# Optimization experiments

Measured on AMD Instinct MI355X. Metric: run time of the kernel, lower is better.

The kernel has to match this reference:

```python
import jax, jax.numpy as jnp
import numpy as np
import math

NUM_HEADS = 16

def setup_inputs() -> dict:
    key = jax.random.key(0)
    ks = jax.random.split(key, 5)
    d_model = 1024
    std = math.sqrt(2.0 / (d_model + d_model))
    x = jax.random.normal(ks[0], (2, 2048, d_model), dtype=jnp.float32)
    Wq = jax.random.normal(ks[1], (d_model, d_model), dtype=jnp.float32) * std
    Wk = jax.random.normal(ks[2], (d_model, d_model), dtype=jnp.float32) * std
    Wv = jax.random.normal(ks[3], (d_model, d_model), dtype=jnp.float32) * std
    Wo = jax.random.normal(ks[4], (d_model, d_model), dtype=jnp.float32) * std
    return {"x": x, "Wq": Wq, "Wk": Wk, "Wv": Wv, "Wo": Wo}

def reference(x, Wq, Wk, Wv, Wo):
    # x: [b, s, d]; W*: [d_out, d_in]
    b, s, d = x.shape
    h = NUM_HEADS
    dh = d // h
    def proj(W):
        y = jnp.einsum('bsd,ed->bse', x, W)           # [b, s, d]
        return y.reshape(b, s, h, dh).transpose(0, 2, 1, 3)  # [b, h, s, dh]
    Q, K, V = proj(Wq), proj(Wk), proj(Wv)
    scale = 1.0 / math.sqrt(dh)
    logits = jnp.einsum('bhqd,bhkd->bhqk', Q, K) * scale  # [b, h, s, s]
    causal = jnp.tril(jnp.ones((s, s), dtype=bool))
    logits = jnp.where(causal, logits, -jnp.inf)
    attn = jax.nn.softmax(logits, axis=-1)
    out = jnp.einsum('bhqk,bhkd->bhqd', attn, V)          # [b, h, s, dh]
    out = out.transpose(0, 2, 1, 3).reshape(b, s, d)
    return jnp.einsum('bsv,dv->bsd', out, Wo)
```

## Files before the change

kernel.cpp:

```cpp
#include <hip/hip_runtime.h>
#include <hip/hip_bf16.h>
#include <math.h>

typedef unsigned short ushort_t;
typedef __attribute__((ext_vector_type(8))) short bf16x8;
typedef __attribute__((ext_vector_type(4))) float f32x4;

#define MFMA16(a,b,c) __builtin_amdgcn_mfma_f32_16x16x32_bf16(a,b,c,0,0,0)
#define QSCALE 0.1803368801111204f

typedef unsigned int u32;
typedef __attribute__((address_space(1))) const u32* gp1_t;
typedef __attribute__((address_space(3))) u32* lp3_t;

__device__ __forceinline__ void async_copy16(void* l, const void* g) {
    __builtin_amdgcn_global_load_lds((gp1_t)g, (lp3_t)l, 16, 0, 0);
}

__device__ __forceinline__ ushort_t f2bf(float f) {
    unsigned u = __float_as_uint(f);
    unsigned r = u + 0x7fffu + ((u >> 16) & 1u);
    return (ushort_t)(r >> 16);
}

__global__ __launch_bounds__(256) void cvt_kernel(
    const float* __restrict__ x,  const float* __restrict__ wq,
    const float* __restrict__ wk, const float* __restrict__ wv,
    const float* __restrict__ wo, ushort_t* __restrict__ dst)
{
    size_t base = ((size_t)blockIdx.x * 256 + threadIdx.x) * 8;
    const float* src; size_t off;
    if      (base < 4194304ul) { src = x;  off = base; }
    else if (base < 5242880ul) { src = wq; off = base - 4194304ul; }
    else if (base < 6291456ul) { src = wk; off = base - 5242880ul; }
    else if (base < 7340032ul) { src = wv; off = base - 6291456ul; }
    else                       { src = wo; off = base - 7340032ul; }
    float4 a = *(const float4*)(src + off);
    float4 b = *(const float4*)(src + off + 4);
    struct alignas(16) U8 { ushort_t v[8]; } o;
    o.v[0]=f2bf(a.x); o.v[1]=f2bf(a.y); o.v[2]=f2bf(a.z); o.v[3]=f2bf(a.w);
    o.v[4]=f2bf(b.x); o.v[5]=f2bf(b.y); o.v[6]=f2bf(b.z); o.v[7]=f2bf(b.w);
    *(U8*)(dst + base) = o;
}

__global__ __launch_bounds__(256) void gemm_bt(
    const ushort_t* __restrict__ A,  const ushort_t* __restrict__ B0,
    const ushort_t* __restrict__ B1, const ushort_t* __restrict__ B2,
    ushort_t* __restrict__ Oq, ushort_t* __restrict__ Ok,
    ushort_t* __restrict__ Ovt, float* __restrict__ Of, int mode_base)
{
    __shared__ ushort_t As[128 * 64];
    __shared__ ushort_t Bs[128 * 64];
    const int t = threadIdx.x, l = t & 63, w = t >> 6;
    const int l4 = l >> 4, lm = l & 15;
    const int wr = w >> 1, wc = w & 1;
    const int n0 = blockIdx.x * 128, m0 = blockIdx.y * 128;
    const int mode = mode_base + blockIdx.z;
    const ushort_t* B = (mode == 1) ? B1 : (mode == 2) ? B2 : B0;

    f32x4 acc[4][4] = {};
    for (int kt = 0; kt < 16; ++kt) {
        const int k0 = kt * 64;
        __syncthreads();
        #pragma unroll
        for (int i = 0; i < 4; ++i) {
            const int row = i * 32 + (t >> 3);
            const int c = (t & 7) ^ (row & 7);
            async_copy16((char*)As + i * 4096 + t * 16,
                         A + (size_t)(m0 + row) * 1024 + k0 + c * 8);
            async_copy16((char*)Bs + i * 4096 + t * 16,
                         B + (size_t)(n0 + row) * 1024 + k0 + c * 8);
        }
        __syncthreads();
        #pragma unroll
        for (int ks = 0; ks < 2; ++ks) {
            bf16x8 af[4], bfr[4];
            #pragma unroll
            for (int mi = 0; mi < 4; ++mi) {
                const int row = wr * 64 + mi * 16 + lm;
                const int ch = l4 + 4 * ks;
                af[mi] = *(const bf16x8*)(As + row * 64 + ((ch ^ (row & 7)) << 3));
            }
            #pragma unroll
            for (int ni = 0; ni < 4; ++ni) {
                const int row = wc * 64 + ni * 16 + lm;
                const int ch = l4 + 4 * ks;
                bfr[ni] = *(const bf16x8*)(Bs + row * 64 + ((ch ^ (row & 7)) << 3));
            }
            #pragma unroll
            for (int mi = 0; mi < 4; ++mi)
                #pragma unroll
                for (int ni = 0; ni < 4; ++ni)
                    acc[mi][ni] = MFMA16(af[mi], bfr[ni], acc[mi][ni]);
        }
    }

    const int mb = m0 + wr * 64, nb = n0 + wc * 64;
    if (mode == 3) {
        #pragma unroll
        for (int mi = 0; mi < 4; ++mi)
            #pragma unroll
            for (int ni = 0; ni < 4; ++ni) {
                const int n = nb + ni * 16 + lm;
                const int mr = mb + mi * 16 + l4 * 4;
                #pragma unroll
                for (int r = 0; r < 4; ++r)
                    Of[(size_t)(mr + r) * 1024 + n] = acc[mi][ni][r];
            }
    } else if (mode == 2) {
        #pragma unroll
        for (int mi = 0; mi < 4; ++mi)
            #pragma unroll
            for (int ni = 0; ni < 4; ++ni) {
                const int n = nb + ni * 16 + lm;
                const int m = mb + mi * 16 + l4 * 4;
                const int b = m >> 11, s = m & 2047, h = n >> 6, d = n & 63;
                ushort4 pk;
                pk.x = f2bf(acc[mi][ni][0]); pk.y = f2bf(acc[mi][ni][1]);
                pk.z = f2bf(acc[mi][ni][2]); pk.w = f2bf(acc[mi][ni][3]);
                *(ushort4*)(Ovt + (((size_t)(b * 16 + h) * 64 + d) * 2048 + s)) = pk;
            }
    } else {
        ushort_t* O = (mode == 0) ? Oq : Ok;
        const float qs = (mode == 0) ? (float)QSCALE : 1.0f;
        #pragma unroll
        for (int mi = 0; mi < 4; ++mi)
            #pragma unroll
            for (int ni = 0; ni < 4; ++ni) {
                const int n = nb + ni * 16 + lm;
                const int h = n >> 6, d = n & 63;
                #pragma unroll
                for (int r = 0; r < 4; ++r) {
                    const int m = mb + mi * 16 + l4 * 4 + r;
                    const int b = m >> 11, s = m & 2047;
                    O[((size_t)(b * 16 + h) * 2048 + s) * 64 + d] =
                        f2bf(acc[mi][ni][r] * qs);
                }
            }
    }
}

template<bool MASK>
__device__ __forceinline__ void attn_tile(
    const ushort_t* Kbuf, const ushort_t* Vbuf, ushort_t* Pw,
    const bf16x8 (&qf)[2], const bf16x8 ones,
    f32x4 (&o)[4], f32x4& ol, float& m_run,
    int kv0, int qrow, int l4, int lm)
{
    f32x4 sf[4] = {};
    #pragma unroll
    for (int ks = 0; ks < 2; ++ks)
        #pragma unroll
        for (int cf = 0; cf < 4; ++cf) {
            const int rowK = cf * 16 + lm;
            const int ch = l4 + 4 * ks;
            bf16x8 kf = *(const bf16x8*)(Kbuf + rowK * 64 + ((ch ^ (rowK & 7)) << 3));
            sf[cf] = MFMA16(kf, qf[ks], sf[cf]);
        }

    float tmax = -1e30f;
    #pragma unroll
    for (int cf = 0; cf < 4; ++cf)
        #pragma unroll
        for (int r = 0; r < 4; ++r) {
            float v = sf[cf][r];
            if (MASK && (kv0 + cf * 16 + l4 * 4 + r > qrow)) v = -30000.f;
            sf[cf][r] = v;
            tmax = fmaxf(tmax, v);
        }
    tmax = fmaxf(tmax, __shfl_xor(tmax, 16));
    tmax = fmaxf(tmax, __shfl_xor(tmax, 32));

    if (!__all(tmax <= m_run + 8.f)) {
        const float mn = fmaxf(m_run, tmax);
        const float alpha = __builtin_amdgcn_exp2f(m_run - mn);
        #pragma unroll
        for (int df = 0; df < 4; ++df)
            #pragma unroll
            for (int r = 0; r < 4; ++r)
                o[df][r] *= alpha;
        #pragma unroll
        for (int r = 0; r < 4; ++r) ol[r] *= alpha;
        m_run = mn;
    }

    #pragma unroll
    for (int cf = 0; cf < 4; ++cf) {
        float p0 = __builtin_amdgcn_exp2f(sf[cf][0] - m_run);
        float p1 = __builtin_amdgcn_exp2f(sf[cf][1] - m_run);
        float p2 = __builtin_amdgcn_exp2f(sf[cf][2] - m_run);
        float p3 = __builtin_amdgcn_exp2f(sf[cf][3] - m_run);
        __hip_bfloat162 b01 = __float22bfloat162_rn(make_float2(p0, p1));
        __hip_bfloat162 b23 = __float22bfloat162_rn(make_float2(p2, p3));
        uint2 pkv;
        __builtin_memcpy(&pkv.x, &b01, 4);
        __builtin_memcpy(&pkv.y, &b23, 4);
        *(uint2*)&Pw[lm * 72 + cf * 16 + l4 * 4] = pkv;
    }

    #pragma unroll
    for (int ks = 0; ks < 2; ++ks) {
        bf16x8 pf = *(const bf16x8*)&Pw[lm * 72 + ks * 32 + l4 * 8];
        #pragma unroll
        for (int df = 0; df < 4; ++df) {
            const int rowV = df * 16 + lm;
            const int ch = l4 + 4 * ks;
            bf16x8 vf = *(const bf16x8*)(Vbuf + rowV * 64 + ((ch ^ (rowV & 7)) << 3));
            o[df] = MFMA16(vf, pf, o[df]);
        }
        ol = MFMA16(ones, pf, ol);
    }
}

__global__ __launch_bounds__(256) void attn_kernel(
    const ushort_t* __restrict__ Qg, const ushort_t* __restrict__ Kg,
    const ushort_t* __restrict__ Vtg, ushort_t* __restrict__ Og)
{
    __shared__ ushort_t Ks[2][64 * 64];
    __shared__ ushort_t Vs[2][64 * 64];
    __shared__ ushort_t Ps[4][16 * 72];
    const int t = threadIdx.x, l = t & 63, w = t >> 6;
    const int l4 = l >> 4, lm = l & 15;
    const int bh = blockIdx.x;
    const int qt = 31 - (int)blockIdx.y;
    const int q0 = qt * 64, q0w = q0 + w * 16;
    const int qrow = q0w + lm;

    bf16x8 qf[2];
    {
        const ushort_t* qp = Qg + ((size_t)bh * 2048 + qrow) * 64 + l4 * 8;
        qf[0] = *(const bf16x8*)qp;
        qf[1] = *(const bf16x8*)(qp + 32);
    }
    bf16x8 ones;
    #pragma unroll
    for (int i = 0; i < 8; ++i) ones[i] = (short)0x3F80;

    f32x4 o[4] = {};
    f32x4 ol = {};
    float m_run = -1e30f;

    const int nkv = qt + 1, last = nkv - 1;
    const int srow = t >> 3, scol = t & 7;
    const int stg_i = (srow >= 32), stg_row = srow & 31;
    const ushort_t* kg0 = Kg + ((size_t)bh * 2048 + srow) * 64 + (scol ^ (srow & 7)) * 8;
    const ushort_t* vg0 = Vtg + ((size_t)bh * 64 + srow) * 2048 + (scol ^ (srow & 7)) * 8;
    (void)stg_i; (void)stg_row;

    async_copy16((char*)&Ks[0][0] + t * 16, kg0);
    async_copy16((char*)&Vs[0][0] + t * 16, vg0);
    async_copy16((char*)&Ks[0][0] + 4096 + t * 16, kg0 + 32 * 64);
    async_copy16((char*)&Vs[0][0] + 4096 + t * 16, vg0 + 32 * 2048);
    __syncthreads();

    for (int kt = 0; kt < last; ++kt) {
        const int cur = kt & 1;
        const size_t koff = (size_t)(kt + 1) * 64 * 64;
        const size_t voff = (size_t)(kt + 1) * 64;
        async_copy16((char*)&Ks[cur ^ 1][0] + t * 16, kg0 + koff);
        async_copy16((char*)&Vs[cur ^ 1][0] + t * 16, vg0 + voff);
        async_copy16((char*)&Ks[cur ^ 1][0] + 4096 + t * 16, kg0 + koff + 32 * 64);
        async_copy16((char*)&Vs[cur ^ 1][0] + 4096 + t * 16, vg0 + voff + 32 * 2048);

        attn_tile<false>(&Ks[cur][0], &Vs[cur][0], &Ps[w][0],
                         qf, ones, o, ol, m_run, kt * 64, qrow, l4, lm);
        __syncthreads();
    }
    attn_tile<true>(&Ks[last & 1][0], &Vs[last & 1][0], &Ps[w][0],
                    qf, ones, o, ol, m_run, last * 64, qrow, l4, lm);

    const int b = bh >> 4, h = bh & 15;
    const float inv = 1.f / ol[0];
    #pragma unroll
    for (int df = 0; df < 4; ++df) {
        ushort4 pk4;
        pk4.x = f2bf(o[df][0] * inv); pk4.y = f2bf(o[df][1] * inv);
        pk4.z = f2bf(o[df][2] * inv); pk4.w = f2bf(o[df][3] * inv);
        *(ushort4*)&Og[((size_t)(b * 2048 + qrow)) * 1024 + h * 64 + df * 16 + l4 * 4] = pk4;
    }
}

extern "C" void kernel_launch(void* const* d_in, const int* in_sizes, int n_in,
                              void* d_out, int out_size, void* d_ws, size_t ws_size,
                              hipStream_t stream)
{
    const float* x  = (const float*)d_in[0];
    const float* Wq = (const float*)d_in[1];
    const float* Wk = (const float*)d_in[2];
    const float* Wv = (const float*)d_in[3];
    const float* Wo = (const float*)d_in[4];

    ushort_t* ws  = (ushort_t*)d_ws;
    ushort_t* xb  = ws;
    ushort_t* wqb = ws + 4194304;
    ushort_t* wkb = ws + 5242880;
    ushort_t* wvb = ws + 6291456;
    ushort_t* wob = ws + 7340032;
    ushort_t* Qw  = ws + 8388608;
    ushort_t* Kw  = ws + 12582912;
    ushort_t* Vtw = ws + 16777216;
    ushort_t* Aow = ws + 20971520;

    cvt_kernel<<<4096, 256, 0, stream>>>(x, Wq, Wk, Wv, Wo, ws);
    gemm_bt<<<dim3(8, 32, 3), 256, 0, stream>>>(xb, wqb, wkb, wvb,
                                                Qw, Kw, Vtw, nullptr, 0);
    attn_kernel<<<dim3(32, 32), 256, 0, stream>>>(Qw, Kw, Vtw, Aow);
    gemm_bt<<<dim3(8, 32, 1), 256, 0, stream>>>(Aow, wob, wob, wob,
                                                nullptr, nullptr, nullptr,
                                                (float*)d_out, 3);
}
```

Measured before the change: 123.7 us.

## Double-buffer GEMM LDS tiles, fuse QKV weights as one N=3072 GEMM, swizzle blocks

The GEMM now double-buffers its A/B LDS tiles, issuing async global-to-LDS loads for the next K slice while MFMAs consume the current one, and needs one barrier per iteration instead of two. The QKV projection treats the three contiguous bf16 weight matrices as a single 3072-row B operand, and picks the output destination from the column offset instead of using blockIdx.z. A block-index swizzle spreads neighbouring workgroups across chunks of the grid to improve L2 reuse. LDS use doubles to 64KB per block, which may reduce occupancy. The single barrier may leave a race: the prefetch into the other buffer is issued before the async loads of the current buffer are confirmed complete.

After: 120.2 us. 2.8% less time.

```diff
diff --git a/kernel.cpp b/kernel.cpp
--- a/kernel.cpp
+++ b/kernel.cpp
@@ -44,34 +44,52 @@
 }
 
 __global__ __launch_bounds__(256) void gemm_bt(
-    const ushort_t* __restrict__ A,  const ushort_t* __restrict__ B0,
-    const ushort_t* __restrict__ B1, const ushort_t* __restrict__ B2,
+    const ushort_t* __restrict__ A, const ushort_t* __restrict__ B,
     ushort_t* __restrict__ Oq, ushort_t* __restrict__ Ok,
-    ushort_t* __restrict__ Ovt, float* __restrict__ Of, int mode_base)
-{
-    __shared__ ushort_t As[128 * 64];
-    __shared__ ushort_t Bs[128 * 64];
+    ushort_t* __restrict__ Ovt, float* __restrict__ Of, int is_out)
+{
+    __shared__ ushort_t As[2][128 * 64];
+    __shared__ ushort_t Bs[2][128 * 64];
     const int t = threadIdx.x, l = t & 63, w = t >> 6;
     const int l4 = l >> 4, lm = l & 15;
     const int wr = w >> 1, wc = w & 1;
-    const int n0 = blockIdx.x * 128, m0 = blockIdx.y * 128;
-    const int mode = mode_base + blockIdx.z;
-    const ushort_t* B = (mode == 1) ? B1 : (mode == 2) ? B2 : B0;
+
+    const int nwg = gridDim.x * gridDim.y;
+    const int orig = (int)blockIdx.y * gridDim.x + (int)blockIdx.x;
+    const int qq = nwg >> 3;
+    const int swz = (orig & 7) * qq + (orig >> 3);
+    const int n0 = (swz % gridDim.x) * 128;
+    const int m0 = (swz / gridDim.x) * 128;
+
+    const int srow = t >> 3, scol = t & 7;
 
     f32x4 acc[4][4] = {};
+
+    #pragma unroll
+    for (int i = 0; i < 4; ++i) {
+        const int row = i * 32 + srow;
+        const int c = scol ^ (row & 7);
+        async_copy16((char*)&As[0][0] + i * 4096 + t * 16,
+                     A + (size_t)(m0 + row) * 1024 + c * 8);
+        async_copy16((char*)&Bs[0][0] + i * 4096 + t * 16,
+                     B + (size_t)(n0 + row) * 1024 + c * 8);
+    }
+    __syncthreads();
+
     for (int kt = 0; kt < 16; ++kt) {
-        const int k0 = kt * 64;
-        __syncthreads();
-        #pragma unroll
-        for (int i = 0; i < 4; ++i) {
-            const int row = i * 32 + (t >> 3);
-            const int c = (t & 7) ^ (row & 7);
-            async_copy16((char*)As + i * 4096 + t * 16,
-                         A + (size_t)(m0 + row) * 1024 + k0 + c * 8);
-            async_copy16((char*)Bs + i * 4096 + t * 16,
-                         B + (size_t)(n0 + row) * 1024 + k0 + c * 8);
-        }
-        __syncthreads();
+        const int cur = kt & 1;
+        if (kt + 1 < 16) {
+            const int k0 = (kt + 1) * 64;
+            #pragma unroll
+            for (int i = 0; i < 4; ++i) {
+                const int row = i * 32 + srow;
+                const int c = scol ^ (row & 7);
+                async_copy16((char*)&As[cur ^ 1][0] + i * 4096 + t * 16,
+                             A + (size_t)(m0 + row) * 1024 + k0 + c * 8);
+                async_copy16((char*)&Bs[cur ^ 1][0] + i * 4096 + t * 16,
+                             B + (size_t)(n0 + row) * 1024 + k0 + c * 8);
+            }
+        }
         #pragma unroll
         for (int ks = 0; ks < 2; ++ks) {
             bf16x8 af[4], bfr[4];
@@ -79,13 +97,13 @@
             for (int mi = 0; mi < 4; ++mi) {
                 const int row = wr * 64 + mi * 16 + lm;
                 const int ch = l4 + 4 * ks;
-                af[mi] = *(const bf16x8*)(As + row * 64 + ((ch ^ (row & 7)) << 3));
+                af[mi] = *(const bf16x8*)(&As[cur][0] + row * 64 + ((ch ^ (row & 7)) << 3));
             }
             #pragma unroll
             for (int ni = 0; ni < 4; ++ni) {
                 const int row = wc * 64 + ni * 16 + lm;
                 const int ch = l4 + 4 * ks;
-                bfr[ni] = *(const bf16x8*)(Bs + row * 64 + ((ch ^ (row & 7)) << 3));
+                bfr[ni] = *(const bf16x8*)(&Bs[cur][0] + row * 64 + ((ch ^ (row & 7)) << 3));
             }
             #pragma unroll
             for (int mi = 0; mi < 4; ++mi)
@@ -93,10 +111,11 @@
                 for (int ni = 0; ni < 4; ++ni)
                     acc[mi][ni] = MFMA16(af[mi], bfr[ni], acc[mi][ni]);
         }
+        __syncthreads();
     }
 
     const int mb = m0 + wr * 64, nb = n0 + wc * 64;
-    if (mode == 3) {
+    if (is_out) {
         #pragma unroll
         for (int mi = 0; mi < 4; ++mi)
             #pragma unroll
@@ -107,27 +126,28 @@
                 for (int r = 0; r < 4; ++r)
                     Of[(size_t)(mr + r) * 1024 + n] = acc[mi][ni][r];
             }
-    } else if (mode == 2) {
+    } else if (nb >= 2048) {
         #pragma unroll
         for (int mi = 0; mi < 4; ++mi)
             #pragma unroll
             for (int ni = 0; ni < 4; ++ni) {
-                const int n = nb + ni * 16 + lm;
+                const int nv = nb - 2048 + ni * 16 + lm;
                 const int m = mb + mi * 16 + l4 * 4;
-                const int b = m >> 11, s = m & 2047, h = n >> 6, d = n & 63;
+                const int b = m >> 11, s = m & 2047, h = nv >> 6, d = nv & 63;
                 ushort4 pk;
                 pk.x = f2bf(acc[mi][ni][0]); pk.y = f2bf(acc[mi][ni][1]);
                 pk.z = f2bf(acc[mi][ni][2]); pk.w = f2bf(acc[mi][ni][3]);
                 *(ushort4*)(Ovt + (((size_t)(b * 16 + h) * 64 + d) * 2048 + s)) = pk;
             }
     } else {
-        ushort_t* O = (mode == 0) ? Oq : Ok;
-        const float qs = (mode == 0) ? (float)QSCALE : 1.0f;
+        ushort_t* O = (nb < 1024) ? Oq : Ok;
+        const float qs = (nb < 1024) ? (float)QSCALE : 1.0f;
+        const int nbase = nb & 1023;
         #pragma unroll
         for (int mi = 0; mi < 4; ++mi)
             #pragma unroll
             for (int ni = 0; ni < 4; ++ni) {
-                const int n = nb + ni * 16 + lm;
+                const int n = nbase + ni * 16 + lm;
                 const int h = n >> 6, d = n & 63;
                 #pragma unroll
                 for (int r = 0; r < 4; ++r) {
@@ -242,10 +262,8 @@
 
     const int nkv = qt + 1, last = nkv - 1;
     const int srow = t >> 3, scol = t & 7;
-    const int stg_i = (srow >= 32), stg_row = srow & 31;
     const ushort_t* kg0 = Kg + ((size_t)bh * 2048 + srow) * 64 + (scol ^ (srow & 7)) * 8;
     const ushort_t* vg0 = Vtg + ((size_t)bh * 64 + srow) * 2048 + (scol ^ (srow & 7)) * 8;
-    (void)stg_i; (void)stg_row;
 
     async_copy16((char*)&Ks[0][0] + t * 16, kg0);
     async_copy16((char*)&Vs[0][0] + t * 16, vg0);
@@ -293,8 +311,6 @@
     ushort_t* ws  = (ushort_t*)d_ws;
     ushort_t* xb  = ws;
     ushort_t* wqb = ws + 4194304;
-    ushort_t* wkb = ws + 5242880;
-    ushort_t* wvb = ws + 6291456;
     ushort_t* wob = ws + 7340032;
     ushort_t* Qw  = ws + 8388608;
     ushort_t* Kw  = ws + 12582912;
@@ -302,10 +318,8 @@
     ushort_t* Aow = ws + 20971520;
 
     cvt_kernel<<<4096, 256, 0, stream>>>(x, Wq, Wk, Wv, Wo, ws);
-    gemm_bt<<<dim3(8, 32, 3), 256, 0, stream>>>(xb, wqb, wkb, wvb,
-                                                Qw, Kw, Vtw, nullptr, 0);
+    gemm_bt<<<dim3(24, 32), 256, 0, stream>>>(xb, wqb, Qw, Kw, Vtw, nullptr, 0);
     attn_kernel<<<dim3(32, 32), 256, 0, stream>>>(Qw, Kw, Vtw, Aow);
-    gemm_bt<<<dim3(8, 32, 1), 256, 0, stream>>>(Aow, wob, wob, wob,
-                                                nullptr, nullptr, nullptr,
-                                                (float*)d_out, 3);
-}
+    gemm_bt<<<dim3(8, 32), 256, 0, stream>>>(Aow, wob, nullptr, nullptr, nullptr,
+                                             (float*)d_out, 1);
+}
```
